# Optimization experiments

Hardware: AMD Instinct MI355X
Metric: run time of the kernel (lower is better)

The kernel has to match this reference:

```python
import jax, jax.numpy as jnp
import numpy as np

N = 100000      # nodes
E = 1600000     # edges (avg degree 16)
D_IN = 128
H = 256
OUT = 20
EPS = 1e-5      # BatchNorm1d default eps


def setup_inputs() -> dict:
    key = jax.random.key(0)
    ks = jax.random.split(key, 16)
    s = 0.05  # keep activations bounded across stacked layers
    x = jax.random.normal(ks[0], (N, D_IN), jnp.float32)
    edge_index = jax.random.randint(ks[1], (2, E), 0, N, dtype=jnp.int32)
    W0 = jax.random.normal(ks[2], (D_IN, H), jnp.float32) * s
    W1 = jax.random.normal(ks[3], (H, H), jnp.float32) * s
    W2 = jax.random.normal(ks[4], (H, H), jnp.float32) * s
    W3 = jax.random.normal(ks[5], (H, OUT), jnp.float32) * s
    b0 = jnp.zeros((H,), jnp.float32)
    b1 = jnp.zeros((H,), jnp.float32)
    b2 = jnp.zeros((H,), jnp.float32)
    b3 = jnp.zeros((OUT,), jnp.float32)
    gamma = jnp.ones((3, H), jnp.float32) + 0.1 * jax.random.normal(ks[6], (3, H), jnp.float32)
    beta = 0.1 * jax.random.normal(ks[7], (3, H), jnp.float32)
    run_mean = 0.05 * jax.random.normal(ks[8], (3, H), jnp.float32)
    run_var = jnp.ones((3, H), jnp.float32) + 0.5 * jax.random.uniform(ks[9], (3, H), jnp.float32)
    return {"x": x, "edge_index": edge_index,
            "W0": W0, "b0": b0, "W1": W1, "b1": b1, "W2": W2, "b2": b2,
            "W3": W3, "b3": b3, "gamma": gamma, "beta": beta,
            "run_mean": run_mean, "run_var": run_var}


def _gcn_aggregate(h, src, dst, dinv_sqrt):
    # PyG GCNConv: add self-loops, sym-normalized scatter-add of projected feats.
    coef = (dinv_sqrt[src] * dinv_sqrt[dst])[:, None]          # [E,1]
    agg = jax.ops.segment_sum(h[src] * coef, dst, num_segments=N)
    # self-loop contribution: norm = deg^-1 for i==j
    return agg + h * (dinv_sqrt * dinv_sqrt)[:, None]


def reference(x, edge_index, W0, b0, W1, b1, W2, b2, W3, b3,
              gamma, beta, run_mean, run_var):
    src, dst = edge_index[0], edge_index[1]
    # degree with self-loops (counted on dst, as PyG does on col index)
    deg = jax.ops.segment_sum(jnp.ones((E,), jnp.float32), dst, num_segments=N) + 1.0
    dinv_sqrt = jax.lax.rsqrt(deg)

    h = x
    for i, (W, b) in enumerate([(W0, b0), (W1, b1), (W2, b2)]):
        h = _gcn_aggregate(h @ W, src, dst, dinv_sqrt) + b
        # BatchNorm1d in eval mode (running stats), then ReLU; dropout is identity in eval
        h = (h - run_mean[i]) * jax.lax.rsqrt(run_var[i] + EPS) * gamma[i] + beta[i]
        h = jax.nn.relu(h)
    h = _gcn_aggregate(h @ W3, src, dst, dinv_sqrt) + b3
    return h
```

## Files before the change

### kernel.cpp

```cpp
#include <hip/hip_runtime.h>
#include <hip/hip_bf16.h>
#include <stdint.h>

#define NN 100000
#define NE 1600000
#define BNEPS 1e-5f
#define NBKT 391
#define NBA  256
#define CHUNK ((NE + NBA - 1) / NBA)

using short8 = __attribute__((ext_vector_type(8))) short;
using f32x4  = __attribute__((ext_vector_type(4))) float;

__device__ __forceinline__ float b2f(ushort u) {
  union { uint32_t u; float f; } c; c.u = ((uint32_t)u) << 16; return c.f;
}
__device__ __forceinline__ ushort f2bf(float f) {
  union { float f; uint32_t u; } c; c.f = f;
  uint32_t r = (c.u + 0x7FFFu + ((c.u >> 16) & 1u)) >> 16;
  return (ushort)r;
}
__device__ __forceinline__ uint pk(float a, float b) {
  return (uint)f2bf(a) | ((uint)f2bf(b) << 16);
}
__device__ __forceinline__ void gload16(const void* g, void* lds) {
  __builtin_amdgcn_global_load_lds((const __attribute__((address_space(1))) void*)g,
                                   (__attribute__((address_space(3))) void*)lds,
                                   16, 0, 0);
}
__device__ __forceinline__ void add16(float* a, uint4 q) {
  a[0] += b2f((ushort)(q.x & 0xFFFF)); a[1] += b2f((ushort)(q.x >> 16));
  a[2] += b2f((ushort)(q.y & 0xFFFF)); a[3] += b2f((ushort)(q.y >> 16));
  a[4] += b2f((ushort)(q.z & 0xFFFF)); a[5] += b2f((ushort)(q.z >> 16));
  a[6] += b2f((ushort)(q.w & 0xFFFF)); a[7] += b2f((ushort)(q.w >> 16));
}
__device__ __forceinline__ void set16(float* a, uint4 q) {
  a[0] = b2f((ushort)(q.x & 0xFFFF)); a[1] = b2f((ushort)(q.x >> 16));
  a[2] = b2f((ushort)(q.y & 0xFFFF)); a[3] = b2f((ushort)(q.y >> 16));
  a[4] = b2f((ushort)(q.z & 0xFFFF)); a[5] = b2f((ushort)(q.z >> 16));
  a[6] = b2f((ushort)(q.w & 0xFFFF)); a[7] = b2f((ushort)(q.w >> 16));
}

__global__ __launch_bounds__(256) void k_hist(const int* __restrict__ dst, int* __restrict__ ghist) {
  __shared__ int h[NBKT];
  for (int t = threadIdx.x; t < NBKT; t += 256) h[t] = 0;
  __syncthreads();
  int e0 = blockIdx.x * CHUNK;
  int e1 = e0 + CHUNK; if (e1 > NE) e1 = NE;
  for (int e = e0 + threadIdx.x; e < e1; e += 256)
    atomicAdd(&h[((uint)dst[e]) >> 8], 1);
  __syncthreads();
  for (int t = threadIdx.x; t < NBKT; t += 256) ghist[t * NBA + blockIdx.x] = h[t];
}

__global__ __launch_bounds__(256) void k_gscanA(const int* __restrict__ ghist, int* __restrict__ gbase,
                                                int* __restrict__ btot) {
  __shared__ int s[256];
  int t = threadIdx.x, b = blockIdx.x;
  int d = ghist[b * NBA + t];
  s[t] = d; __syncthreads();
  int val = d;
  for (int sh = 1; sh < 256; sh <<= 1) {
    int tv = (t >= sh) ? s[t - sh] : 0;
    __syncthreads();
    val += tv; s[t] = val;
    __syncthreads();
  }
  gbase[b * NBA + t] = val - d;
  if (t == 255) btot[b] = val;
}

__global__ __launch_bounds__(512) void k_bscan(const int* __restrict__ btot, int* __restrict__ bbase,
                                               int* __restrict__ offs) {
  __shared__ int s[512];
  int t = threadIdx.x;
  int d = (t < NBKT) ? btot[t] : 0;
  s[t] = d; __syncthreads();
  int val = d;
  for (int sh = 1; sh < 512; sh <<= 1) {
    int tv = (t >= sh) ? s[t - sh] : 0;
    __syncthreads();
    val += tv; s[t] = val;
    __syncthreads();
  }
  if (t < NBKT) bbase[t] = val - d;
  if (t == 0) offs[NN] = NE;
}

__global__ __launch_bounds__(256) void k_scatter(const int* __restrict__ src, const int* __restrict__ dst,
                                                 const int* __restrict__ bbase, const int* __restrict__ gbase,
                                                 uint* __restrict__ bpack) {
  __shared__ int lbase[NBKT];
  for (int t = threadIdx.x; t < NBKT; t += 256)
    lbase[t] = bbase[t] + gbase[t * NBA + blockIdx.x];
  __syncthreads();
  int e0 = blockIdx.x * CHUNK;
  int e1 = e0 + CHUNK; if (e1 > NE) e1 = NE;
  for (int e = e0 + threadIdx.x; e < e1; e += 256) {
    int d = dst[e];
    int pos = atomicAdd(&lbase[((uint)d) >> 8], 1);
    bpack[pos] = ((uint)(d & 255) << 17) | (uint)src[e];
  }
}

__global__ __launch_bounds__(256) void k_bucketB(const uint* __restrict__ bpack, const int* __restrict__ btot,
                                                 const int* __restrict__ bbase, int* __restrict__ csrc,
                                                 int* __restrict__ offs, float* __restrict__ dinv) {
  __shared__ int hist[256];
  __shared__ int sc[256];
  __shared__ int loc[256];
  int b = blockIdx.x, t = threadIdx.x;
  int cnt = btot[b], base = bbase[b];
  const uint* bp = bpack + base;
  hist[t] = 0; __syncthreads();
  for (int i = t; i < cnt; i += 256) atomicAdd(&hist[bp[i] >> 17], 1);
  __syncthreads();
  int d = hist[t];
  sc[t] = d; __syncthreads();
  int val = d;
  for (int sh = 1; sh < 256; sh <<= 1) {
    int tv = (t >= sh) ? sc[t - sh] : 0;
    __syncthreads();
    val += tv; sc[t] = val;
    __syncthreads();
  }
  loc[t] = val - d;
  int n = b * 256 + t;
  if (n < NN) {
    offs[n] = base + val - d;
    dinv[n] = rsqrtf((float)d + 1.0f);
  }
  __syncthreads();
  for (int i = t; i < cnt; i += 256) {
    uint p = bp[i];
    int l = p >> 17, s = p & 0x1FFFF;
    int pos = atomicAdd(&loc[l], 1);
    csrc[base + pos] = s;
  }
}

__global__ __launch_bounds__(256) void k_prep(
    const float* __restrict__ W0, const float* __restrict__ W1, const float* __restrict__ W2,
    const float* __restrict__ W3, const float* __restrict__ b0, const float* __restrict__ b1,
    const float* __restrict__ b2, const float* __restrict__ gamma, const float* __restrict__ beta,
    const float* __restrict__ rm, const float* __restrict__ rv,
    ushort* __restrict__ W0t, ushort* __restrict__ W1t, ushort* __restrict__ W2t,
    ushort* __restrict__ W3t, float* __restrict__ bnA, float* __restrict__ bnB) {
  int tid = blockIdx.x * blockDim.x + threadIdx.x;
  int nthr = gridDim.x * blockDim.x;
  for (int i = tid; i < 256 * 128; i += nthr) { int m = i >> 7, k = i & 127; W0t[i] = f2bf(W0[k * 256 + m]); }
  for (int i = tid; i < 256 * 256; i += nthr) {
    int m = i >> 8, k = i & 255;
    W1t[i] = f2bf(W1[k * 256 + m]);
    W2t[i] = f2bf(W2[k * 256 + m]);
  }
  for (int i = tid; i < 32 * 256; i += nthr) {
    int m = i >> 8, k = i & 255;
    W3t[i] = (m < 20) ? f2bf(W3[k * 20 + m]) : (ushort)0;
  }
  for (int i = tid; i < 3 * 256; i += nthr) {
    int l = i >> 8, c = i & 255;
    float A = gamma[i] * rsqrtf(rv[i] + BNEPS);
    float bb = (l == 0) ? b0[c] : (l == 1) ? b1[c] : b2[c];
    bnA[i] = A;
    bnB[i] = (bb - rm[i]) * A + beta[i];
  }
}

__global__ __launch_bounds__(256) void k_convx(const float4* __restrict__ x, uint2* __restrict__ xb,
                                               const float* __restrict__ dinv) {
  int stride = gridDim.x * blockDim.x;
  const int n4 = NN * 128 / 4;
  for (int i = blockIdx.x * blockDim.x + threadIdx.x; i < n4; i += stride) {
    float4 f = x[i];
    float dv = dinv[i >> 5];
    uint2 o;
    o.x = pk(f.x * dv, f.y * dv);
    o.y = pk(f.z * dv, f.w * dv);
    xb[i] = o;
  }
}


__global__ __launch_bounds__(256) void k_agg256(const ushort* __restrict__ Z,
                                                const int* __restrict__ offs, const int* __restrict__ csrc,
                                                const float* __restrict__ dinv, ushort* __restrict__ Outb) {
  int wave = threadIdx.x >> 6, lane = threadIdx.x & 63;
  int v = blockIdx.x * 4 + wave;
  if (v >= NN) return;
  float dv = dinv[v];
  int p = lane >> 5, fl = lane & 31;
  const uint4* Z4 = reinterpret_cast<const uint4*>(Z);
  float acc[8];
  if (p == 0) {
    set16(acc, Z4[(size_t)v * 32 + fl]);
  } else {
#pragma unroll
    for (int j = 0; j < 8; ++j) acc[j] = 0.0f;
  }
  int e1 = offs[v + 1];
  int e = offs[v] + p;
  for (; e + 6 < e1; e += 8) {
    int u0 = csrc[e], u1 = csrc[e + 2], u2 = csrc[e + 4], u3 = csrc[e + 6];
    uint4 q0 = Z4[(size_t)u0 * 32 + fl];
    uint4 q1 = Z4[(size_t)u1 * 32 + fl];
    uint4 q2 = Z4[(size_t)u2 * 32 + fl];
    uint4 q3 = Z4[(size_t)u3 * 32 + fl];
    add16(acc, q0); add16(acc, q1); add16(acc, q2); add16(acc, q3);
  }
  for (; e < e1; e += 2) add16(acc, Z4[(size_t)csrc[e] * 32 + fl]);
#pragma unroll
  for (int j = 0; j < 8; ++j) acc[j] += __shfl_xor(acc[j], 32);
  int o = p * 4;
  uint2 w;
  w.x = pk(acc[o + 0] * dv, acc[o + 1] * dv);
  w.y = pk(acc[o + 2] * dv, acc[o + 3] * dv);
  reinterpret_cast<uint2*>(Outb)[(size_t)v * 64 + fl * 2 + p] = w;
}

__global__ __launch_bounds__(256) void k_agg128(const ushort* __restrict__ Z,
                                                const int* __restrict__ offs, const int* __restrict__ csrc,
                                                const float* __restrict__ dinv, ushort* __restrict__ Outb) {
  int wave = threadIdx.x >> 6, lane = threadIdx.x & 63;
  int v = blockIdx.x * 4 + wave;
  if (v >= NN) return;
  float dv = dinv[v];
  int q = lane >> 4, fl = lane & 15;
  const uint4* Z4 = reinterpret_cast<const uint4*>(Z);
  float acc[8];
  if (q == 0) {
    set16(acc, Z4[(size_t)v * 16 + fl]);
  } else {
#pragma unroll
    for (int j = 0; j < 8; ++j) acc[j] = 0.0f;
  }
  int e1 = offs[v + 1];
  int e = offs[v] + q;
  for (; e + 12 < e1; e += 16) {
    int u0 = csrc[e], u1 = csrc[e + 4], u2 = csrc[e + 8], u3 = csrc[e + 12];
    uint4 q0 = Z4[(size_t)u0 * 16 + fl];
    uint4 q1 = Z4[(size_t)u1 * 16 + fl];
    uint4 q2 = Z4[(size_t)u2 * 16 + fl];
    uint4 q3 = Z4[(size_t)u3 * 16 + fl];
    add16(acc, q0); add16(acc, q1); add16(acc, q2); add16(acc, q3);
  }
  for (; e < e1; e += 4) add16(acc, Z4[(size_t)csrc[e] * 16 + fl]);
#pragma unroll
  for (int j = 0; j < 8; ++j) {
    acc[j] += __shfl_xor(acc[j], 16);
    acc[j] += __shfl_xor(acc[j], 32);
  }
  uint w = pk(acc[2 * q] * dv, acc[2 * q + 1] * dv);
  reinterpret_cast<uint*>(Outb)[(size_t)v * 64 + fl * 4 + q] = w;
}

__global__ __launch_bounds__(256) void k_aggfin(const ushort* __restrict__ Z,
                                                const int* __restrict__ offs, const int* __restrict__ csrc,
                                                const float* __restrict__ dinv, const float* __restrict__ b3,
                                                float* __restrict__ out) {
  int wave = threadIdx.x >> 6, lane = threadIdx.x & 63;
  int v = blockIdx.x * 4 + wave;
  if (v >= NN) return;
  float dv = dinv[v];
  int s = lane >> 3, fl = lane & 7;
  const uint2* Z2 = reinterpret_cast<const uint2*>(Z);
  float acc[4];
  if (s == 0) {
    uint2 qq = Z2[(size_t)v * 8 + fl];
    acc[0] = b2f((ushort)(qq.x & 0xFFFF)); acc[1] = b2f((ushort)(qq.x >> 16));
    acc[2] = b2f((ushort)(qq.y & 0xFFFF)); acc[3] = b2f((ushort)(qq.y >> 16));
  } else {
    acc[0] = acc[1] = acc[2] = acc[3] = 0.0f;
  }
  int e1 = offs[v + 1];
  int e = offs[v] + s;
  for (; e + 8 < e1; e += 16) {
    int u0 = csrc[e], u1 = csrc[e + 8];
    uint2 q0 = Z2[(size_t)u0 * 8 + fl];
    uint2 q1 = Z2[(size_t)u1 * 8 + fl];
    acc[0] += b2f((ushort)(q0.x & 0xFFFF)) + b2f((ushort)(q1.x & 0xFFFF));
    acc[1] += b2f((ushort)(q0.x >> 16))    + b2f((ushort)(q1.x >> 16));
    acc[2] += b2f((ushort)(q0.y & 0xFFFF)) + b2f((ushort)(q1.y & 0xFFFF));
    acc[3] += b2f((ushort)(q0.y >> 16))    + b2f((ushort)(q1.y >> 16));
  }
  for (; e < e1; e += 8) {
    uint2 qq = Z2[(size_t)csrc[e] * 8 + fl];
    acc[0] += b2f((ushort)(qq.x & 0xFFFF)); acc[1] += b2f((ushort)(qq.x >> 16));
    acc[2] += b2f((ushort)(qq.y & 0xFFFF)); acc[3] += b2f((ushort)(qq.y >> 16));
  }
#pragma unroll
  for (int j = 0; j < 4; ++j) {
    acc[j] += __shfl_xor(acc[j], 8);
    acc[j] += __shfl_xor(acc[j], 16);
    acc[j] += __shfl_xor(acc[j], 32);
  }
  if (s == 0 && fl < 5) {
    float4 w;
    w.x = acc[0] * dv + b3[fl * 4 + 0];
    w.y = acc[1] * dv + b3[fl * 4 + 1];
    w.z = acc[2] * dv + b3[fl * 4 + 2];
    w.w = acc[3] * dv + b3[fl * 4 + 3];
    *reinterpret_cast<float4*>(out + (size_t)v * 20 + fl * 4) = w;
  }
}

template<int KTOT, int BN, bool EPI, bool SCALE>
__global__ __launch_bounds__(256) void k_gemm(const ushort* __restrict__ A,
                                              const ushort* __restrict__ Bt,
                                              ushort* __restrict__ Out,
                                              const float* __restrict__ bnA,
                                              const float* __restrict__ bnB,
                                              const float* __restrict__ dinv, int outW) {
  constexpr int BM = 128, BK = 64;
  constexpr int WN = (BN == 128) ? 64 : 16;
  constexpr int WM = 64;
  constexpr int FM = WM / 16, FN = WN / 16;
  __shared__ ushort Alds[BM * BK];
  __shared__ ushort Blds[BN * BK];
  int tid = threadIdx.x;
  int lane = tid & 63;
  int wave = tid >> 6;
  int wm = wave >> 1, wn = wave & 1;
  size_t row0 = (size_t)blockIdx.x * BM;
  int col0 = blockIdx.y * BN;

  f32x4 acc[FM][FN];
#pragma unroll
  for (int i = 0; i < FM; ++i)
#pragma unroll
    for (int j = 0; j < FN; ++j)
#pragma unroll
      for (int r = 0; r < 4; ++r) acc[i][j][r] = 0.0f;

  for (int k0 = 0; k0 < KTOT; k0 += BK) {
#pragma unroll
    for (int is = 0; is < 4; ++is) {
      int idx = is * 256 + tid;
      int r = idx >> 3, c = idx & 7;
      size_t gr = row0 + r; if (gr >= NN) gr = NN - 1;
      gload16(A + gr * KTOT + k0 + c * 8, &Alds[(size_t)(idx & ~63) * 8]);
    }
#pragma unroll
    for (int is = 0; is < BN / 32; ++is) {
      int idx = is * 256 + tid;
      int r = idx >> 3, c = idx & 7;
      gload16(Bt + (size_t)(col0 + r) * KTOT + k0 + c * 8, &Blds[(size_t)(idx & ~63) * 8]);
    }
    __syncthreads();
#pragma unroll
    for (int kk = 0; kk < BK; kk += 32) {
      short8 af[FM]; short8 bfr[FN];
#pragma unroll
      for (int fm = 0; fm < FM; ++fm)
        af[fm] = *reinterpret_cast<const short8*>(&Alds[(wm * WM + fm * 16 + (lane & 15)) * BK + kk + (lane >> 4) * 8]);
#pragma unroll
      for (int fn = 0; fn < FN; ++fn)
        bfr[fn] = *reinterpret_cast<const short8*>(&Blds[(wn * WN + fn * 16 + (lane & 15)) * BK + kk + (lane >> 4) * 8]);
#pragma unroll
      for (int fm = 0; fm < FM; ++fm)
#pragma unroll
        for (int fn = 0; fn < FN; ++fn)
          acc[fm][fn] = __builtin_amdgcn_mfma_f32_16x16x32_bf16(af[fm], bfr[fn], acc[fm][fn], 0, 0, 0);
    }
    __syncthreads();
  }

  int lr = (lane >> 4) * 4, lc = lane & 15;
#pragma unroll
  for (int fm = 0; fm < FM; ++fm) {
#pragma unroll
    for (int r = 0; r < 4; ++r) {
      size_t grow = row0 + wm * WM + fm * 16 + lr + r;
      if (grow >= NN) continue;
      float ds = 1.0f;
      if constexpr (SCALE) ds = dinv[grow];
#pragma unroll
      for (int fn = 0; fn < FN; ++fn) {
        int gcol = col0 + wn * WN + fn * 16 + lc;
        float v = acc[fm][fn][r];
        if constexpr (EPI) v = fmaxf(v * bnA[gcol] + bnB[gcol], 0.0f);
        if constexpr (SCALE) v *= ds;
        Out[grow * outW + gcol] = f2bf(v);
      }
    }
  }
}

extern "C" void kernel_launch(void* const* d_in, const int* in_sizes, int n_in,
                              void* d_out, int out_size, void* d_ws, size_t ws_size,
                              hipStream_t stream) {
  (void)in_sizes; (void)n_in; (void)out_size; (void)ws_size;
  const float* x     = (const float*)d_in[0];
  const int*   ei    = (const int*)d_in[1];
  const float* W0    = (const float*)d_in[2];
  const float* b0    = (const float*)d_in[3];
  const float* W1    = (const float*)d_in[4];
  const float* b1    = (const float*)d_in[5];
  const float* W2    = (const float*)d_in[6];
  const float* b2    = (const float*)d_in[7];
  const float* W3    = (const float*)d_in[8];
  const float* b3    = (const float*)d_in[9];
  const float* gamma = (const float*)d_in[10];
  const float* beta  = (const float*)d_in[11];
  const float* rm    = (const float*)d_in[12];
  const float* rv    = (const float*)d_in[13];
  const int* src = ei;
  const int* dst = ei + NE;
  float* out = (float*)d_out;

  char* ws = (char*)d_ws;
  size_t off = 0;
  auto alloc = [&](size_t bytes) -> void* {
    void* p = ws + off; off += (bytes + 255) & ~(size_t)255; return p;
  };
  int*    ghist = (int*)alloc((size_t)NBKT * NBA * 4);
  int*    gbase = (int*)alloc((size_t)NBKT * NBA * 4);
  int*    btot  = (int*)alloc(NBKT * 4);
  int*    bbase = (int*)alloc(NBKT * 4);
  uint*   bpack = (uint*)alloc((size_t)NE * 4);
  int*    offs  = (int*)alloc((NN + 1) * (size_t)4);
  int*    csrc  = (int*)alloc((size_t)NE * 4);
  float*  dinv  = (float*)alloc(NN * 4);
  ushort* W0t   = (ushort*)alloc(256 * 128 * 2);
  ushort* W1t   = (ushort*)alloc(256 * 256 * 2);
  ushort* W2t   = (ushort*)alloc(256 * 256 * 2);
  ushort* W3t   = (ushort*)alloc(32 * 256 * 2);
  float*  bnA   = (float*)alloc(3 * 256 * 4);
  float*  bnB   = (float*)alloc(3 * 256 * 4);
  ushort* bufS  = (ushort*)alloc((size_t)NN * 128 * 2);
  ushort* bufA  = (ushort*)alloc((size_t)NN * 256 * 2);
  ushort* bufB  = (ushort*)alloc((size_t)NN * 256 * 2);

  k_hist<<<NBA, 256, 0, stream>>>(dst, ghist);
  k_gscanA<<<NBKT, 256, 0, stream>>>(ghist, gbase, btot);
  k_bscan<<<1, 512, 0, stream>>>(btot, bbase, offs);
  k_scatter<<<NBA, 256, 0, stream>>>(src, dst, bbase, gbase, bpack);
  k_bucketB<<<NBKT, 256, 0, stream>>>(bpack, btot, bbase, csrc, offs, dinv);
  k_prep<<<256, 256, 0, stream>>>(W0, W1, W2, W3, b0, b1, b2, gamma, beta, rm, rv,
                                  W0t, W1t, W2t, W3t, bnA, bnB);
  k_convx<<<2048, 256, 0, stream>>>((const float4*)x, (uint2*)bufS, dinv);

  const int aggBlocks = (NN + 3) / 4;
  dim3 gMain((NN + 127) / 128, 2);
  dim3 gLast((NN + 127) / 128, 1);

  k_agg128<<<aggBlocks, 256, 0, stream>>>(bufS, offs, csrc, dinv, bufA);
  k_gemm<128, 128, true, true><<<gMain, 256, 0, stream>>>(bufA, W0t, bufB, bnA, bnB, dinv, 256);
  k_agg256<<<aggBlocks, 256, 0, stream>>>(bufB, offs, csrc, dinv, bufA);
  k_gemm<256, 128, true, true><<<gMain, 256, 0, stream>>>(bufA, W1t, bufB, bnA + 256, bnB + 256, dinv, 256);
  k_agg256<<<aggBlocks, 256, 0, stream>>>(bufB, offs, csrc, dinv, bufA);
  k_gemm<256, 128, true, false><<<gMain, 256, 0, stream>>>(bufA, W2t, bufB, bnA + 512, bnB + 512, nullptr, 256);
  k_gemm<256, 32, false, true><<<gLast, 256, 0, stream>>>(bufB, W3t, bufS, nullptr, nullptr, dinv, 32);
  k_aggfin<<<aggBlocks, 256, 0, stream>>>(bufS, offs, csrc, dinv, b3, out);
}
```

Before: 526.4 us.

## Add double-buffered swizzled-LDS MFMA GEMM for hidden layers and swap grid order

Introduces k_gemm2, which double-buffers A and B tiles in LDS so the global loads for the next K-slice overlap the MFMA work on the current one. LDS placement is XOR-swizzled to avoid bank conflicts. The grid is reordered so the two column blocks sharing a row tile launch next to each other, which should improve L2 reuse of A rows. The cost is twice the LDS per block, which may lower occupancy, and the epilogue writes scalar bf16 values that may coalesce less well.

Result: slower. 538.9 us (+2.4%).

```diff
diff --git a/kernel.cpp b/kernel.cpp
--- a/kernel.cpp
+++ b/kernel.cpp
@@ -301,6 +301,103 @@
     w.z = acc[2] * dv + b3[fl * 4 + 2];
     w.w = acc[3] * dv + b3[fl * 4 + 3];
     *reinterpret_cast<float4*>(out + (size_t)v * 20 + fl * 4) = w;
+  }
+}
+
+template<int KT, bool EPI, bool SCALE>
+__global__ __launch_bounds__(256) void k_gemm2(const ushort* __restrict__ A,
+                                               const ushort* __restrict__ Bt,
+                                               ushort* __restrict__ Out,
+                                               const float* __restrict__ bnA,
+                                               const float* __restrict__ bnB,
+                                               const float* __restrict__ dinv) {
+  constexpr int BK = 64;
+  constexpr int NT = KT / BK;
+  __shared__ ushort Ald[2][128 * 64];
+  __shared__ ushort Bld[2][128 * 64];
+  int tid = threadIdx.x;
+  int lane = tid & 63;
+  int wave = tid >> 6;
+  int wm = wave >> 1, wn = wave & 1;
+  size_t row0 = (size_t)blockIdx.y * 128;
+  int col0 = blockIdx.x * 128;
+  int laneLo = lane & 15, laneHi = lane >> 4;
+
+  f32x4 acc[4][4];
+#pragma unroll
+  for (int i = 0; i < 4; ++i)
+#pragma unroll
+    for (int j = 0; j < 4; ++j)
+#pragma unroll
+      for (int r = 0; r < 4; ++r) acc[i][j][r] = 0.0f;
+
+  auto stage = [&](int buf, int k0) {
+#pragma unroll
+    for (int is = 0; is < 4; ++is) {
+      int idx = is * 256 + tid;
+      int r = idx >> 3, c = idx & 7;
+      size_t gr = row0 + r; if (gr >= NN) gr = NN - 1;
+      gload16(A + gr * KT + k0 + ((c ^ (r & 7)) << 3), &Ald[buf][(idx & ~63) * 8]);
+    }
+#pragma unroll
+    for (int is = 0; is < 4; ++is) {
+      int idx = is * 256 + tid;
+      int r = idx >> 3, c = idx & 7;
+      gload16(Bt + (size_t)(col0 + r) * KT + k0 + ((c ^ (r & 7)) << 3), &Bld[buf][(idx & ~63) * 8]);
+    }
+  };
+
+  stage(0, 0);
+  asm volatile("s_waitcnt vmcnt(0)" ::: "memory");
+  __builtin_amdgcn_s_barrier();
+
+  for (int t = 0; t < NT; ++t) {
+    int cur = t & 1;
+    if (t + 1 < NT) stage(cur ^ 1, (t + 1) * BK);
+#pragma unroll
+    for (int kk = 0; kk < BK; kk += 32) {
+      short8 af[4]; short8 bf[4];
+      int slotBase = kk >> 3;
+#pragma unroll
+      for (int fm = 0; fm < 4; ++fm) {
+        int R = wm * 64 + fm * 16 + laneLo;
+        int sl = (slotBase + laneHi) ^ (R & 7);
+        af[fm] = *reinterpret_cast<const short8*>(&Ald[cur][R * 64 + sl * 8]);
+      }
+#pragma unroll
+      for (int fn = 0; fn < 4; ++fn) {
+        int R = wn * 64 + fn * 16 + laneLo;
+        int sl = (slotBase + laneHi) ^ (R & 7);
+        bf[fn] = *reinterpret_cast<const short8*>(&Bld[cur][R * 64 + sl * 8]);
+      }
+#pragma unroll
+      for (int fm = 0; fm < 4; ++fm)
+#pragma unroll
+        for (int fn = 0; fn < 4; ++fn)
+          acc[fm][fn] = __builtin_amdgcn_mfma_f32_16x16x32_bf16(af[fm], bf[fn], acc[fm][fn], 0, 0, 0);
+    }
+    asm volatile("s_waitcnt vmcnt(0)" ::: "memory");
+    __builtin_amdgcn_s_barrier();
+  }
+
+  int lr = laneHi * 4, lc = laneLo;
+#pragma unroll
+  for (int fm = 0; fm < 4; ++fm) {
+#pragma unroll
+    for (int r = 0; r < 4; ++r) {
+      size_t grow = row0 + wm * 64 + fm * 16 + lr + r;
+      if (grow >= NN) continue;
+      float ds = 1.0f;
+      if constexpr (SCALE) ds = dinv[grow];
+#pragma unroll
+      for (int fn = 0; fn < 4; ++fn) {
+        int gcol = col0 + wn * 64 + fn * 16 + lc;
+        float v = acc[fm][fn][r];
+        if constexpr (EPI) v = fmaxf(v * bnA[gcol] + bnB[gcol], 0.0f);
+        if constexpr (SCALE) v *= ds;
+        Out[grow * 256 + gcol] = f2bf(v);
+      }
+    }
   }
 }
 
@@ -441,15 +538,15 @@
   k_convx<<<2048, 256, 0, stream>>>((const float4*)x, (uint2*)bufS, dinv);
 
   const int aggBlocks = (NN + 3) / 4;
-  dim3 gMain((NN + 127) / 128, 2);
+  dim3 gMain(2, (NN + 127) / 128);
   dim3 gLast((NN + 127) / 128, 1);
 
   k_agg128<<<aggBlocks, 256, 0, stream>>>(bufS, offs, csrc, dinv, bufA);
-  k_gemm<128, 128, true, true><<<gMain, 256, 0, stream>>>(bufA, W0t, bufB, bnA, bnB, dinv, 256);
+  k_gemm2<128, true, true><<<gMain, 256, 0, stream>>>(bufA, W0t, bufB, bnA, bnB, dinv);
   k_agg256<<<aggBlocks, 256, 0, stream>>>(bufB, offs, csrc, dinv, bufA);
-  k_gemm<256, 128, true, true><<<gMain, 256, 0, stream>>>(bufA, W1t, bufB, bnA + 256, bnB + 256, dinv, 256);
+  k_gemm2<256, true, true><<<gMain, 256, 0, stream>>>(bufA, W1t, bufB, bnA + 256, bnB + 256, dinv);
   k_agg256<<<aggBlocks, 256, 0, stream>>>(bufB, offs, csrc, dinv, bufA);
-  k_gemm<256, 128, true, false><<<gMain, 256, 0, stream>>>(bufA, W2t, bufB, bnA + 512, bnB + 512, nullptr, 256);
+  k_gemm2<256, true, false><<<gMain, 256, 0, stream>>>(bufA, W2t, bufB, bnA + 512, bnB + 512, nullptr);
   k_gemm<256, 32, false, true><<<gLast, 256, 0, stream>>>(bufB, W3t, bufS, nullptr, nullptr, dinv, 32);
   k_aggfin<<<aggBlocks, 256, 0, stream>>>(bufS, offs, csrc, dinv, b3, out);
 }
```

## Split 256-wide aggregation across eight feature slices per node

Applied to the files above, without the earlier changes.

Replaces the 256-feature aggregation kernel with one that launches eight blocks per group of nodes. Each block handles a 32-feature slice, using 4-byte loads per lane and four edge slots per wave, and reduces the partial sums with shuffles. The aim is more parallelism and occupancy for the gather. The cost is narrower loads, eight-fold redundant reads of the offsets and indices, and only a quarter of lanes writing output.

Result: slower. 992.6 us (+88.6%).

```diff
diff --git a/kernel.cpp b/kernel.cpp
--- a/kernel.cpp
+++ b/kernel.cpp
@@ -182,40 +182,47 @@
 }
 
 
-__global__ __launch_bounds__(256) void k_agg256(const ushort* __restrict__ Z,
-                                                const int* __restrict__ offs, const int* __restrict__ csrc,
-                                                const float* __restrict__ dinv, ushort* __restrict__ Outb) {
+__global__ __launch_bounds__(256) void k_agg256s(const ushort* __restrict__ Z,
+                                                 const int* __restrict__ offs, const int* __restrict__ csrc,
+                                                 const float* __restrict__ dinv, ushort* __restrict__ Outb) {
   int wave = threadIdx.x >> 6, lane = threadIdx.x & 63;
-  int v = blockIdx.x * 4 + wave;
+  int s = blockIdx.x & 7;
+  int v = (blockIdx.x >> 3) * 4 + wave;
   if (v >= NN) return;
   float dv = dinv[v];
-  int p = lane >> 5, fl = lane & 31;
-  const uint4* Z4 = reinterpret_cast<const uint4*>(Z);
-  float acc[8];
-  if (p == 0) {
-    set16(acc, Z4[(size_t)v * 32 + fl]);
+  int slot = lane >> 4, fl = lane & 15;
+  const uint* Zu = reinterpret_cast<const uint*>(Z);
+  int base = s * 16 + fl;
+  float a0, a1;
+  if (slot == 0) {
+    uint q = Zu[(size_t)v * 128 + base];
+    a0 = b2f((ushort)(q & 0xFFFF));
+    a1 = b2f((ushort)(q >> 16));
   } else {
-#pragma unroll
-    for (int j = 0; j < 8; ++j) acc[j] = 0.0f;
+    a0 = 0.0f; a1 = 0.0f;
   }
   int e1 = offs[v + 1];
-  int e = offs[v] + p;
-  for (; e + 6 < e1; e += 8) {
-    int u0 = csrc[e], u1 = csrc[e + 2], u2 = csrc[e + 4], u3 = csrc[e + 6];
-    uint4 q0 = Z4[(size_t)u0 * 32 + fl];
-    uint4 q1 = Z4[(size_t)u1 * 32 + fl];
-    uint4 q2 = Z4[(size_t)u2 * 32 + fl];
-    uint4 q3 = Z4[(size_t)u3 * 32 + fl];
-    add16(acc, q0); add16(acc, q1); add16(acc, q2); add16(acc, q3);
-  }
-  for (; e < e1; e += 2) add16(acc, Z4[(size_t)csrc[e] * 32 + fl]);
-#pragma unroll
-  for (int j = 0; j < 8; ++j) acc[j] += __shfl_xor(acc[j], 32);
-  int o = p * 4;
-  uint2 w;
-  w.x = pk(acc[o + 0] * dv, acc[o + 1] * dv);
-  w.y = pk(acc[o + 2] * dv, acc[o + 3] * dv);
-  reinterpret_cast<uint2*>(Outb)[(size_t)v * 64 + fl * 2 + p] = w;
+  int e = offs[v] + slot;
+  for (; e + 12 < e1; e += 16) {
+    int u0 = csrc[e], u1 = csrc[e + 4], u2 = csrc[e + 8], u3 = csrc[e + 12];
+    uint q0 = Zu[(size_t)u0 * 128 + base];
+    uint q1 = Zu[(size_t)u1 * 128 + base];
+    uint q2 = Zu[(size_t)u2 * 128 + base];
+    uint q3 = Zu[(size_t)u3 * 128 + base];
+    a0 += (b2f((ushort)(q0 & 0xFFFF)) + b2f((ushort)(q1 & 0xFFFF)))
+        + (b2f((ushort)(q2 & 0xFFFF)) + b2f((ushort)(q3 & 0xFFFF)));
+    a1 += (b2f((ushort)(q0 >> 16)) + b2f((ushort)(q1 >> 16)))
+        + (b2f((ushort)(q2 >> 16)) + b2f((ushort)(q3 >> 16)));
+  }
+  for (; e < e1; e += 4) {
+    uint q = Zu[(size_t)csrc[e] * 128 + base];
+    a0 += b2f((ushort)(q & 0xFFFF));
+    a1 += b2f((ushort)(q >> 16));
+  }
+  a0 += __shfl_xor(a0, 16); a0 += __shfl_xor(a0, 32);
+  a1 += __shfl_xor(a1, 16); a1 += __shfl_xor(a1, 32);
+  if (slot == 0)
+    reinterpret_cast<uint*>(Outb)[(size_t)v * 128 + base] = pk(a0 * dv, a1 * dv);
 }
 
 __global__ __launch_bounds__(256) void k_agg128(const ushort* __restrict__ Z,
@@ -441,14 +448,15 @@
   k_convx<<<2048, 256, 0, stream>>>((const float4*)x, (uint2*)bufS, dinv);
 
   const int aggBlocks = (NN + 3) / 4;
+  const int aggSBlocks = aggBlocks * 8;
   dim3 gMain((NN + 127) / 128, 2);
   dim3 gLast((NN + 127) / 128, 1);
 
   k_agg128<<<aggBlocks, 256, 0, stream>>>(bufS, offs, csrc, dinv, bufA);
   k_gemm<128, 128, true, true><<<gMain, 256, 0, stream>>>(bufA, W0t, bufB, bnA, bnB, dinv, 256);
-  k_agg256<<<aggBlocks, 256, 0, stream>>>(bufB, offs, csrc, dinv, bufA);
+  k_agg256s<<<aggSBlocks, 256, 0, stream>>>(bufB, offs, csrc, dinv, bufA);
   k_gemm<256, 128, true, true><<<gMain, 256, 0, stream>>>(bufA, W1t, bufB, bnA + 256, bnB + 256, dinv, 256);
-  k_agg256<<<aggBlocks, 256, 0, stream>>>(bufB, offs, csrc, dinv, bufA);
+  k_agg256s<<<aggSBlocks, 256, 0, stream>>>(bufB, offs, csrc, dinv, bufA);
   k_gemm<256, 128, true, false><<<gMain, 256, 0, stream>>>(bufA, W2t, bufB, bnA + 512, bnB + 512, nullptr, 256);
   k_gemm<256, 32, false, true><<<gLast, 256, 0, stream>>>(bufB, W3t, bufS, nullptr, nullptr, dinv, 32);
   k_aggfin<<<aggBlocks, 256, 0, stream>>>(bufS, offs, csrc, dinv, b3, out);
```
